# Kernel optimization log

Measured on AMD Instinct MI355X. Metric: run time of the kernel, lower is better.

## Reference

```python
import jax, jax.numpy as jnp
import numpy as np

N_NODES = 40000
N_EDGES = 640000
N_GRAPHS = 400
HID = 64
EDGE_DIM = 4
NUM_CLASSES = 12
EPS_BN = 1e-5


def _glorot(key, shape, fan_in, fan_out):
    s = jnp.sqrt(6.0 / (fan_in + fan_out)).astype(jnp.float32)
    return jax.random.uniform(key, shape, jnp.float32, -s, s)


def setup_inputs() -> dict:
    key = jax.random.key(0)
    ks = jax.random.split(key, 24)
    x = jax.random.normal(ks[0], (N_NODES, 2), jnp.float32)
    edge_index = jax.random.randint(ks[1], (2, N_EDGES), 0, N_NODES, jnp.int32)
    edge_attr = jax.random.normal(ks[2], (N_EDGES, EDGE_DIM), jnp.float32)
    batch = jnp.sort(jax.random.randint(ks[3], (N_NODES,), 0, N_GRAPHS, jnp.int32))
    H1, C1 = 4, HID            # conv1: heads=4, out=64, concat -> 256
    H2, C2 = 2, HID * 2        # conv2: heads=2, out=128, mean -> 128
    d1 = H1 * C1               # 256
    d2 = H2 * C2               # 256 (pre-mean), post 128
    return {
        "x": x, "edge_index": edge_index, "edge_attr": edge_attr, "batch": batch,
        # conv1 params
        "Wl1": _glorot(ks[4], (2, d1), 2, d1), "bl1": jnp.zeros((d1,), jnp.float32),
        "Wr1": _glorot(ks[5], (2, d1), 2, d1), "br1": jnp.zeros((d1,), jnp.float32),
        "We1": _glorot(ks[6], (EDGE_DIM, d1), EDGE_DIM, d1),
        "att1": _glorot(ks[7], (H1, C1), C1, 1),
        "bias1": jnp.zeros((d1,), jnp.float32),
        "g1": jnp.ones((d1,), jnp.float32), "be1": jnp.zeros((d1,), jnp.float32),
        # conv2 params
        "Wl2": _glorot(ks[8], (d1, d2), d1, d2), "bl2": jnp.zeros((d2,), jnp.float32),
        "Wr2": _glorot(ks[9], (d1, d2), d1, d2), "br2": jnp.zeros((d2,), jnp.float32),
        "We2": _glorot(ks[10], (EDGE_DIM, d2), EDGE_DIM, d2),
        "att2": _glorot(ks[11], (H2, C2), C2, 1),
        "bias2": jnp.zeros((C2,), jnp.float32),
        "g2": jnp.ones((C2,), jnp.float32), "be2": jnp.zeros((C2,), jnp.float32),
        # MLP head
        "W_lin1": _glorot(ks[12], (C2, HID), C2, HID), "b_lin1": jnp.zeros((HID,), jnp.float32),
        "W_lin2": _glorot(ks[13], (HID, NUM_CLASSES), HID, NUM_CLASSES),
        "b_lin2": jnp.zeros((NUM_CLASSES,), jnp.float32),
    }


def gatv2(x, src, dst, ea, Wl, bl, Wr, br, We, att, bias, heads, out_ch, concat):
    N = x.shape[0]
    xl = (x @ Wl + bl).reshape(N, heads, out_ch)   # source transform
    xr = (x @ Wr + br).reshape(N, heads, out_ch)   # target transform
    ee = (ea @ We).reshape(-1, heads, out_ch)      # edge features
    z = jax.nn.leaky_relu(xl[src] + xr[dst] + ee, 0.2)  # [E,H,C]
    e = jnp.einsum('ehc,hc->eh', z, att)
    # segment softmax over edges grouped by destination node
    m = jax.ops.segment_max(e, dst, num_segments=N)
    ex = jnp.exp(e - m[dst])
    den = jax.ops.segment_sum(ex, dst, num_segments=N)
    alpha = ex / (den[dst] + 1e-16)
    out = jax.ops.segment_sum(xl[src] * alpha[:, :, None], dst, num_segments=N)
    out = out.reshape(N, heads * out_ch) if concat else out.mean(axis=1)
    return out + bias


def batchnorm(x, g, b):
    mu = x.mean(axis=0)
    var = x.var(axis=0)
    return (x - mu) * jax.lax.rsqrt(var + EPS_BN) * g + b


def reference(x, edge_index, edge_attr, batch,
              Wl1, bl1, Wr1, br1, We1, att1, bias1, g1, be1,
              Wl2, bl2, Wr2, br2, We2, att2, bias2, g2, be2,
              W_lin1, b_lin1, W_lin2, b_lin2):
    src, dst = edge_index[0], edge_index[1]
    h = gatv2(x, src, dst, edge_attr, Wl1, bl1, Wr1, br1, We1, att1, bias1, 4, HID, True)
    h = jax.nn.elu(batchnorm(h, g1, be1))
    h = gatv2(h, src, dst, edge_attr, Wl2, bl2, Wr2, br2, We2, att2, bias2, 2, HID * 2, False)
    h = jax.nn.elu(batchnorm(h, g2, be2))
    # global mean pool per graph
    s = jax.ops.segment_sum(h, batch, num_segments=N_GRAPHS)
    cnt = jax.ops.segment_sum(jnp.ones((h.shape[0],), h.dtype), batch, num_segments=N_GRAPHS)
    h = s / jnp.maximum(cnt, 1.0)[:, None]
    h = jax.nn.elu(h @ W_lin1 + b_lin1)
    return h @ W_lin2 + b_lin2
```

## Files before the change

### kernel.cpp

```cpp
#include <hip/hip_runtime.h>
#include <math.h>

#define NN_ 40000
#define NE_ 640000
#define NG_ 400
#define NBLK_SCAN 157
#define NBP 1024
#define NB2 32

typedef unsigned short ushort_t;
typedef __attribute__((ext_vector_type(8))) short bf16x8;
typedef __attribute__((ext_vector_type(4))) float f32x4;

__device__ int    g_deg[NN_];
__device__ int    g_rowstart[NN_ + 1];
__device__ int    g_cursor[NN_];
__device__ int    g_srccsr[NE_];
__device__ float4 g_eacsr[NE_];
__device__ int    g_bsum[NBLK_SCAN], g_boff[NBLK_SCAN];
__device__ ushort_t g_xl1[(size_t)NN_ * 256];
__device__ ushort_t g_xr1[(size_t)NN_ * 256];
__device__ ushort_t g_xl2[(size_t)NN_ * 256];
__device__ ushort_t g_xr2[(size_t)NN_ * 256];
__device__ float  g_h1[(size_t)NN_ * 256];
__device__ ushort_t g_h1b[(size_t)NN_ * 256];
__device__ ushort_t g_wl2t[256 * 256];
__device__ ushort_t g_wr2t[256 * 256];
__device__ float  g_h2[(size_t)NN_ * 128];
__device__ float  g_part_s[NBP][256];
__device__ float  g_part_q[NBP][256];
__device__ float  g_p2_s[NB2][256];
__device__ float  g_p2_q[NB2][256];
__device__ float  g_scale[256], g_shift[256];
__device__ float  g_pool[NG_ * 128];
__device__ int    g_count[NG_];

__device__ __forceinline__ float bflo(unsigned int q) { return __uint_as_float(q << 16); }
__device__ __forceinline__ float bfhi(unsigned int q) { return __uint_as_float(q & 0xFFFF0000u); }
__device__ __forceinline__ unsigned int f2bf(float f) {
    unsigned int u = __float_as_uint(f);
    return (u + 0x7FFFu + ((u >> 16) & 1u)) >> 16;
}
__device__ __forceinline__ unsigned int pack2(float a, float b) {
    return f2bf(a) | (f2bf(b) << 16);
}

__global__ void k_zero() {
    int i = blockIdx.x * blockDim.x + threadIdx.x;
    int stride = gridDim.x * blockDim.x;
    for (int j = i; j < NN_; j += stride) g_deg[j] = 0;
}

__global__ void k_hist(const int* __restrict__ dst) {
    int e = blockIdx.x * blockDim.x + threadIdx.x;
    if (e < NE_) atomicAdd(&g_deg[dst[e]], 1);
}

__global__ void k_scan1() {
    __shared__ int sd[256];
    int b = blockIdx.x, t = threadIdx.x, i = b * 256 + t;
    int v = (i < NN_) ? g_deg[i] : 0;
    sd[t] = v;
    __syncthreads();
    for (int off = 1; off < 256; off <<= 1) {
        int tv = (t >= off) ? sd[t - off] : 0;
        __syncthreads();
        sd[t] += tv;
        __syncthreads();
    }
    if (i < NN_) g_rowstart[i] = sd[t] - v;
    if (t == 255) g_bsum[b] = sd[255];
}

__global__ void k_scan2() {
    __shared__ int sd[256];
    int t = threadIdx.x;
    int v = (t < NBLK_SCAN) ? g_bsum[t] : 0;
    sd[t] = v;
    __syncthreads();
    for (int off = 1; off < 256; off <<= 1) {
        int tv = (t >= off) ? sd[t - off] : 0;
        __syncthreads();
        sd[t] += tv;
        __syncthreads();
    }
    if (t < NBLK_SCAN) g_boff[t] = sd[t] - v;
    if (t == 255) g_rowstart[NN_] = sd[255];
}

__global__ void k_scan3() {
    int i = blockIdx.x * blockDim.x + threadIdx.x;
    if (i < NN_) {
        int r = g_rowstart[i] + g_boff[i >> 8];
        g_rowstart[i] = r;
        g_cursor[i] = r;
    }
}

__global__ void k_scatter(const int* __restrict__ src, const int* __restrict__ dst,
                          const float* __restrict__ ea) {
    int e = blockIdx.x * blockDim.x + threadIdx.x;
    if (e < NE_) {
        int pos = atomicAdd(&g_cursor[dst[e]], 1);
        g_srccsr[pos] = src[e];
        g_eacsr[pos] = reinterpret_cast<const float4*>(ea)[e];
    }
}

__global__ void k_xform1(const float* __restrict__ x,
                         const float* __restrict__ Wl, const float* __restrict__ bl,
                         const float* __restrict__ Wr, const float* __restrict__ br) {
    int n = blockIdx.x * 4 + (threadIdx.x >> 6);
    int lane = threadIdx.x & 63;
    if (n >= NN_) return;
    float x0 = x[2 * n], x1 = x[2 * n + 1];
    int c4 = lane * 4;
    float l0 = x0 * Wl[c4 + 0] + x1 * Wl[256 + c4 + 0] + bl[c4 + 0];
    float l1 = x0 * Wl[c4 + 1] + x1 * Wl[256 + c4 + 1] + bl[c4 + 1];
    float l2 = x0 * Wl[c4 + 2] + x1 * Wl[256 + c4 + 2] + bl[c4 + 2];
    float l3 = x0 * Wl[c4 + 3] + x1 * Wl[256 + c4 + 3] + bl[c4 + 3];
    float r0 = x0 * Wr[c4 + 0] + x1 * Wr[256 + c4 + 0] + br[c4 + 0];
    float r1 = x0 * Wr[c4 + 1] + x1 * Wr[256 + c4 + 1] + br[c4 + 1];
    float r2 = x0 * Wr[c4 + 2] + x1 * Wr[256 + c4 + 2] + br[c4 + 2];
    float r3 = x0 * Wr[c4 + 3] + x1 * Wr[256 + c4 + 3] + br[c4 + 3];
    *reinterpret_cast<uint2*>(g_xl1 + (size_t)n * 256 + c4) = make_uint2(pack2(l0, l1), pack2(l2, l3));
    *reinterpret_cast<uint2*>(g_xr1 + (size_t)n * 256 + c4) = make_uint2(pack2(r0, r1), pack2(r2, r3));
}

template <int LAYER>
__global__ void k_gat(const float* __restrict__ att, const float* __restrict__ We,
                      const float* __restrict__ bias) {
    constexpr int C = (LAYER == 1) ? 64 : 128;
    constexpr int GL = C / 4;
    const ushort_t* __restrict__ xl = (LAYER == 1) ? g_xl1 : g_xl2;
    const ushort_t* __restrict__ xr = (LAYER == 1) ? g_xr1 : g_xr2;
    float* __restrict__ hout = (LAYER == 1) ? g_h1 : g_h2;

    int wv = threadIdx.x >> 6, lane = threadIdx.x & 63;
    int n = blockIdx.x * 4 + wv;
    if (n >= NN_) return;
    int c4 = lane * 4;

    float a0 = att[c4], a1 = att[c4 + 1], a2c = att[c4 + 2], a3 = att[c4 + 3];
    float we00 = We[c4], we01 = We[c4 + 1], we02 = We[c4 + 2], we03 = We[c4 + 3];
    float we10 = We[256 + c4], we11 = We[256 + c4 + 1], we12 = We[256 + c4 + 2], we13 = We[256 + c4 + 3];
    float we20 = We[512 + c4], we21 = We[512 + c4 + 1], we22 = We[512 + c4 + 2], we23 = We[512 + c4 + 3];
    float we30 = We[768 + c4], we31 = We[768 + c4 + 1], we32 = We[768 + c4 + 2], we33 = We[768 + c4 + 3];
    uint2 xq = *reinterpret_cast<const uint2*>(xr + (size_t)n * 256 + c4);
    float xr0 = bflo(xq.x), xr1 = bfhi(xq.x), xr2 = bflo(xq.y), xr3 = bfhi(xq.y);

    int s0 = g_rowstart[n];
    int d = g_rowstart[n + 1] - s0;

    float mrun = -INFINITY, den = 0.f;
    float acc0 = 0.f, acc1 = 0.f, acc2 = 0.f, acc3 = 0.f;

    int   sA = 0;
    float4 eaA = make_float4(0.f, 0.f, 0.f, 0.f);
    uint2 rowA = make_uint2(0u, 0u);
    if (d > 0) {
        sA = g_srccsr[s0];
        eaA = g_eacsr[s0];
        rowA = *reinterpret_cast<const uint2*>(xl + (size_t)sA * 256 + c4);
    }
    for (int i = 0; i < d; ++i) {
        int   sB = sA;
        float4 eaB = eaA;
        uint2 rowB = rowA;
        if (i + 1 < d) {
            sB = g_srccsr[s0 + i + 1];
            eaB = g_eacsr[s0 + i + 1];
            rowB = *reinterpret_cast<const uint2*>(xl + (size_t)sB * 256 + c4);
        }
        float xl0 = bflo(rowA.x), xl1 = bfhi(rowA.x), xl2 = bflo(rowA.y), xl3 = bfhi(rowA.y);
        float z0 = xl0 + xr0 + eaA.x * we00 + eaA.y * we10 + eaA.z * we20 + eaA.w * we30;
        float z1 = xl1 + xr1 + eaA.x * we01 + eaA.y * we11 + eaA.z * we21 + eaA.w * we31;
        float z2 = xl2 + xr2 + eaA.x * we02 + eaA.y * we12 + eaA.z * we22 + eaA.w * we32;
        float z3 = xl3 + xr3 + eaA.x * we03 + eaA.y * we13 + eaA.z * we23 + eaA.w * we33;
        z0 = fmaxf(z0, 0.2f * z0); z1 = fmaxf(z1, 0.2f * z1);
        z2 = fmaxf(z2, 0.2f * z2); z3 = fmaxf(z3, 0.2f * z3);
        float t = z0 * a0 + z1 * a1 + z2 * a2c + z3 * a3;
#pragma unroll
        for (int off = 1; off < GL; off <<= 1) t += __shfl_xor(t, off);
        if (__ballot(t > mrun) == 0ULL) {
            float w = __expf(t - mrun);
            den += w;
            acc0 = fmaf(w, xl0, acc0);
            acc1 = fmaf(w, xl1, acc1);
            acc2 = fmaf(w, xl2, acc2);
            acc3 = fmaf(w, xl3, acc3);
        } else {
            float mnew = fmaxf(mrun, t);
            float scl = __expf(mrun - mnew);
            float w = __expf(t - mnew);
            den = den * scl + w;
            acc0 = acc0 * scl + w * xl0;
            acc1 = acc1 * scl + w * xl1;
            acc2 = acc2 * scl + w * xl2;
            acc3 = acc3 * scl + w * xl3;
            mrun = mnew;
        }
        sA = sB; eaA = eaB; rowA = rowB;
    }
    float inv = 1.f / (den + 1e-16f);
    if (LAYER == 1) {
        float4 o = make_float4(acc0 * inv + bias[c4 + 0], acc1 * inv + bias[c4 + 1],
                               acc2 * inv + bias[c4 + 2], acc3 * inv + bias[c4 + 3]);
        *reinterpret_cast<float4*>(hout + (size_t)n * 256 + c4) = o;
    } else {
        float v0 = acc0 * inv, v1 = acc1 * inv, v2 = acc2 * inv, v3 = acc3 * inv;
        float u0 = __shfl_xor(v0, 32), u1 = __shfl_xor(v1, 32);
        float u2 = __shfl_xor(v2, 32), u3 = __shfl_xor(v3, 32);
        if (lane < 32) {
            float4 o = make_float4(0.5f * (v0 + u0) + bias[c4 + 0],
                                   0.5f * (v1 + u1) + bias[c4 + 1],
                                   0.5f * (v2 + u2) + bias[c4 + 2],
                                   0.5f * (v3 + u3) + bias[c4 + 3]);
            *reinterpret_cast<float4*>(hout + (size_t)n * 128 + c4) = o;
        }
    }
}

template <int C>
__global__ void k_bn_stats() {
    const float* h = (C == 256) ? (const float*)g_h1 : (const float*)g_h2;
    int c = threadIdx.x;
    float s = 0.f, ss = 0.f;
    for (int r = blockIdx.x; r < NN_; r += NBP) {
        float v = h[(size_t)r * C + c];
        s += v; ss += v * v;
    }
    g_part_s[blockIdx.x][c] = s;
    g_part_q[blockIdx.x][c] = ss;
}

template <int C>
__global__ void k_bn_reduce() {
    int c = threadIdx.x;
    int b = blockIdx.x;
    float s = 0.f, ss = 0.f;
    for (int p = b; p < NBP; p += NB2) {
        s += g_part_s[p][c];
        ss += g_part_q[p][c];
    }
    g_p2_s[b][c] = s;
    g_p2_q[b][c] = ss;
}

template <int C>
__global__ void k_bn_finalize(const float* __restrict__ g, const float* __restrict__ b) {
    int c = threadIdx.x;
    float s = 0.f, ss = 0.f;
#pragma unroll
    for (int p = 0; p < NB2; ++p) {
        s += g_p2_s[p][c];
        ss += g_p2_q[p][c];
    }
    float mu = s / (float)NN_;
    float var = ss / (float)NN_ - mu * mu;
    float sc = g[c] * rsqrtf(var + 1e-5f);
    g_scale[c] = sc;
    g_shift[c] = b[c] - mu * sc;
}

__global__ void k_bn_apply1() {
    int i = blockIdx.x * blockDim.x + threadIdx.x;
    int stride = gridDim.x * blockDim.x;
    for (int j8 = i; j8 < NN_ * 32; j8 += stride) {
        size_t base = (size_t)j8 * 8;
        int c0 = (int)(base & 255);
        float4 v0 = *reinterpret_cast<const float4*>(g_h1 + base);
        float4 v1 = *reinterpret_cast<const float4*>(g_h1 + base + 4);
        float e[8];
        e[0] = v0.x * g_scale[c0 + 0] + g_shift[c0 + 0];
        e[1] = v0.y * g_scale[c0 + 1] + g_shift[c0 + 1];
        e[2] = v0.z * g_scale[c0 + 2] + g_shift[c0 + 2];
        e[3] = v0.w * g_scale[c0 + 3] + g_shift[c0 + 3];
        e[4] = v1.x * g_scale[c0 + 4] + g_shift[c0 + 4];
        e[5] = v1.y * g_scale[c0 + 5] + g_shift[c0 + 5];
        e[6] = v1.z * g_scale[c0 + 6] + g_shift[c0 + 6];
        e[7] = v1.w * g_scale[c0 + 7] + g_shift[c0 + 7];
#pragma unroll
        for (int q = 0; q < 8; ++q) e[q] = e[q] > 0.f ? e[q] : expm1f(e[q]);
        uint4 o = make_uint4(pack2(e[0], e[1]), pack2(e[2], e[3]),
                             pack2(e[4], e[5]), pack2(e[6], e[7]));
        *reinterpret_cast<uint4*>(g_h1b + base) = o;
    }
}

__global__ void k_wconv(const float* __restrict__ Wl, const float* __restrict__ Wr) {
    int n = blockIdx.x, k = threadIdx.x;
    g_wl2t[n * 256 + k] = (ushort_t)f2bf(Wl[(size_t)k * 256 + n]);
    g_wr2t[n * 256 + k] = (ushort_t)f2bf(Wr[(size_t)k * 256 + n]);
}

__global__ __launch_bounds__(256) void k_gemm2(const float* __restrict__ bl,
                                               const float* __restrict__ br) {
    __shared__ ushort_t As[128][40];
    __shared__ ushort_t Bs[2][64][40];
    int tid = threadIdx.x;
    int w = tid >> 6, lane = tid & 63;
    int m0 = blockIdx.x * 128, n0 = blockIdx.y * 64;

    f32x4 acc[2][4][2] = {};

    for (int k0 = 0; k0 < 256; k0 += 32) {
#pragma unroll
        for (int c = tid; c < 512; c += 256) {
            int row = c >> 2, seg = c & 3;
            int gr = m0 + row; gr = gr < NN_ ? gr : NN_ - 1;
            uint4 v = *reinterpret_cast<const uint4*>(g_h1b + (size_t)gr * 256 + k0 + seg * 8);
            *reinterpret_cast<uint4*>(&As[row][seg * 8]) = v;
        }
        {
            int row = tid >> 2, seg = tid & 3;
            uint4 v0 = *reinterpret_cast<const uint4*>(g_wl2t + (size_t)(n0 + row) * 256 + k0 + seg * 8);
            *reinterpret_cast<uint4*>(&Bs[0][row][seg * 8]) = v0;
            uint4 v1 = *reinterpret_cast<const uint4*>(g_wr2t + (size_t)(n0 + row) * 256 + k0 + seg * 8);
            *reinterpret_cast<uint4*>(&Bs[1][row][seg * 8]) = v1;
        }
        __syncthreads();
        int kb = (lane >> 4) * 8;
        bf16x8 a0 = *reinterpret_cast<const bf16x8*>(&As[w * 32 + (lane & 15)][kb]);
        bf16x8 a1 = *reinterpret_cast<const bf16x8*>(&As[w * 32 + 16 + (lane & 15)][kb]);
        bf16x8 b[4][2];
#pragma unroll
        for (int ni = 0; ni < 4; ++ni) {
            b[ni][0] = *reinterpret_cast<const bf16x8*>(&Bs[0][ni * 16 + (lane & 15)][kb]);
            b[ni][1] = *reinterpret_cast<const bf16x8*>(&Bs[1][ni * 16 + (lane & 15)][kb]);
        }
#pragma unroll
        for (int ni = 0; ni < 4; ++ni) {
#pragma unroll
            for (int mat = 0; mat < 2; ++mat) {
                acc[0][ni][mat] = __builtin_amdgcn_mfma_f32_16x16x32_bf16(a0, b[ni][mat], acc[0][ni][mat], 0, 0, 0);
                acc[1][ni][mat] = __builtin_amdgcn_mfma_f32_16x16x32_bf16(a1, b[ni][mat], acc[1][ni][mat], 0, 0, 0);
            }
        }
        __syncthreads();
    }
#pragma unroll
    for (int mat = 0; mat < 2; ++mat) {
        const float* bb = mat ? br : bl;
        ushort_t* outp = mat ? g_xr2 : g_xl2;
#pragma unroll
        for (int ni = 0; ni < 4; ++ni) {
            int gcol = n0 + ni * 16 + (lane & 15);
            float bv = bb[gcol];
#pragma unroll
            for (int mi = 0; mi < 2; ++mi) {
#pragma unroll
                for (int r = 0; r < 4; ++r) {
                    int grow = m0 + w * 32 + mi * 16 + (lane >> 4) * 4 + r;
                    if (grow < NN_)
                        outp[(size_t)grow * 256 + gcol] = (ushort_t)f2bf(acc[mi][ni][mat][r] + bv);
                }
            }
        }
    }
}

__global__ void k_pool2(const int* __restrict__ batch) {
    int g = blockIdx.x, t = threadIdx.x;
    __shared__ int sbeg, send;
    if (t == 0) {
        int lo = 0, hi = NN_;
        while (lo < hi) { int mid = (lo + hi) >> 1; if (batch[mid] < g) lo = mid + 1; else hi = mid; }
        sbeg = lo;
    }
    if (t == 1) {
        int lo = 0, hi = NN_;
        while (lo < hi) { int mid = (lo + hi) >> 1; if (batch[mid] <= g) lo = mid + 1; else hi = mid; }
        send = lo;
    }
    __syncthreads();
    int beg = sbeg, end = send;
    float sc = g_scale[t], sh = g_shift[t];
    float acc = 0.f;
    for (int n = beg; n < end; ++n) {
        float v = g_h2[(size_t)n * 128 + t] * sc + sh;
        acc += (v > 0.f ? v : expm1f(v));
    }
    g_pool[g * 128 + t] = acc;
    if (t == 0) g_count[g] = end - beg;
}

__global__ void k_head(const float* __restrict__ W1, const float* __restrict__ b1,
                       const float* __restrict__ W2, const float* __restrict__ b2,
                       float* __restrict__ out) {
    int g = blockIdx.x, t = threadIdx.x;
    __shared__ float p[128], hm[64];
    float cnt = fmaxf((float)g_count[g], 1.f);
    float inv = 1.f / cnt;
    p[t] = g_pool[g * 128 + t] * inv;
    p[t + 64] = g_pool[g * 128 + 64 + t] * inv;
    __syncthreads();
    float a = b1[t];
    for (int k = 0; k < 128; ++k) a += p[k] * W1[k * 64 + t];
    hm[t] = a > 0.f ? a : expm1f(a);
    __syncthreads();
    if (t < 12) {
        float o = b2[t];
        for (int k = 0; k < 64; ++k) o += hm[k] * W2[k * 12 + t];
        out[g * 12 + t] = o;
    }
}

extern "C" void kernel_launch(void* const* d_in, const int* in_sizes, int n_in,
                              void* d_out, int out_size, void* d_ws, size_t ws_size,
                              hipStream_t stream) {
    const float* x     = (const float*)d_in[0];
    const int*   ei    = (const int*)d_in[1];
    const float* ea    = (const float*)d_in[2];
    const int*   batch = (const int*)d_in[3];
    const float* Wl1   = (const float*)d_in[4];
    const float* bl1   = (const float*)d_in[5];
    const float* Wr1   = (const float*)d_in[6];
    const float* br1   = (const float*)d_in[7];
    const float* We1   = (const float*)d_in[8];
    const float* att1  = (const float*)d_in[9];
    const float* bias1 = (const float*)d_in[10];
    const float* g1    = (const float*)d_in[11];
    const float* be1   = (const float*)d_in[12];
    const float* Wl2   = (const float*)d_in[13];
    const float* bl2   = (const float*)d_in[14];
    const float* Wr2   = (const float*)d_in[15];
    const float* br2   = (const float*)d_in[16];
    const float* We2   = (const float*)d_in[17];
    const float* att2  = (const float*)d_in[18];
    const float* bias2 = (const float*)d_in[19];
    const float* g2    = (const float*)d_in[20];
    const float* be2   = (const float*)d_in[21];
    const float* Wlin1 = (const float*)d_in[22];
    const float* blin1 = (const float*)d_in[23];
    const float* Wlin2 = (const float*)d_in[24];
    const float* blin2 = (const float*)d_in[25];
    float* out = (float*)d_out;
    const int* src = ei;
    const int* dst = ei + NE_;

    k_zero<<<256, 256, 0, stream>>>();
    k_hist<<<2500, 256, 0, stream>>>(dst);
    k_scan1<<<NBLK_SCAN, 256, 0, stream>>>();
    k_scan2<<<1, 256, 0, stream>>>();
    k_scan3<<<NBLK_SCAN, 256, 0, stream>>>();
    k_scatter<<<2500, 256, 0, stream>>>(src, dst, ea);

    k_xform1<<<10000, 256, 0, stream>>>(x, Wl1, bl1, Wr1, br1);
    k_wconv<<<256, 256, 0, stream>>>(Wl2, Wr2);
    k_gat<1><<<10000, 256, 0, stream>>>(att1, We1, bias1);
    k_bn_stats<256><<<NBP, 256, 0, stream>>>();
    k_bn_reduce<256><<<NB2, 256, 0, stream>>>();
    k_bn_finalize<256><<<1, 256, 0, stream>>>(g1, be1);
    k_bn_apply1<<<2048, 256, 0, stream>>>();

    k_gemm2<<<dim3(313, 4), 256, 0, stream>>>(bl2, br2);

    k_gat<2><<<10000, 256, 0, stream>>>(att2, We2, bias2);
    k_bn_stats<128><<<NBP, 128, 0, stream>>>();
    k_bn_reduce<128><<<NB2, 128, 0, stream>>>();
    k_bn_finalize<128><<<1, 128, 0, stream>>>(g2, be2);

    k_pool2<<<NG_, 128, 0, stream>>>(batch);
    k_head<<<NG_, 64, 0, stream>>>(Wlin1, blin1, Wlin2, blin2, out);
}
```

Measured before the change: 473.2 us.

## Fuse layer-1 linear transform into GAT gather and merge BN2 finalize with pool and head

Layer 1 no longer materializes the 256-wide bf16 xl1/xr1 tensors. Each edge now gathers only the 2-float input x of its source node and recomputes the linear projection in registers. This removes a large write plus random 512-byte gathers per edge, at the cost of a few extra FMAs. Separately, the BN2 finalize, pooling and MLP head are merged into one kernel, which cuts two launches and some intermediate global buffers but repeats the BN stat reduction in every block.

```diff
diff --git a/kernel.cpp b/kernel.cpp
--- a/kernel.cpp
+++ b/kernel.cpp
@@ -18,8 +18,6 @@
 __device__ int    g_srccsr[NE_];
 __device__ float4 g_eacsr[NE_];
 __device__ int    g_bsum[NBLK_SCAN], g_boff[NBLK_SCAN];
-__device__ ushort_t g_xl1[(size_t)NN_ * 256];
-__device__ ushort_t g_xr1[(size_t)NN_ * 256];
 __device__ ushort_t g_xl2[(size_t)NN_ * 256];
 __device__ ushort_t g_xr2[(size_t)NN_ * 256];
 __device__ float  g_h1[(size_t)NN_ * 256];
@@ -32,8 +30,6 @@
 __device__ float  g_p2_s[NB2][256];
 __device__ float  g_p2_q[NB2][256];
 __device__ float  g_scale[256], g_shift[256];
-__device__ float  g_pool[NG_ * 128];
-__device__ int    g_count[NG_];
 
 __device__ __forceinline__ float bflo(unsigned int q) { return __uint_as_float(q << 16); }
 __device__ __forceinline__ float bfhi(unsigned int q) { return __uint_as_float(q & 0xFFFF0000u); }
@@ -107,33 +103,13 @@
     }
 }
 
-__global__ void k_xform1(const float* __restrict__ x,
-                         const float* __restrict__ Wl, const float* __restrict__ bl,
-                         const float* __restrict__ Wr, const float* __restrict__ br) {
-    int n = blockIdx.x * 4 + (threadIdx.x >> 6);
-    int lane = threadIdx.x & 63;
-    if (n >= NN_) return;
-    float x0 = x[2 * n], x1 = x[2 * n + 1];
-    int c4 = lane * 4;
-    float l0 = x0 * Wl[c4 + 0] + x1 * Wl[256 + c4 + 0] + bl[c4 + 0];
-    float l1 = x0 * Wl[c4 + 1] + x1 * Wl[256 + c4 + 1] + bl[c4 + 1];
-    float l2 = x0 * Wl[c4 + 2] + x1 * Wl[256 + c4 + 2] + bl[c4 + 2];
-    float l3 = x0 * Wl[c4 + 3] + x1 * Wl[256 + c4 + 3] + bl[c4 + 3];
-    float r0 = x0 * Wr[c4 + 0] + x1 * Wr[256 + c4 + 0] + br[c4 + 0];
-    float r1 = x0 * Wr[c4 + 1] + x1 * Wr[256 + c4 + 1] + br[c4 + 1];
-    float r2 = x0 * Wr[c4 + 2] + x1 * Wr[256 + c4 + 2] + br[c4 + 2];
-    float r3 = x0 * Wr[c4 + 3] + x1 * Wr[256 + c4 + 3] + br[c4 + 3];
-    *reinterpret_cast<uint2*>(g_xl1 + (size_t)n * 256 + c4) = make_uint2(pack2(l0, l1), pack2(l2, l3));
-    *reinterpret_cast<uint2*>(g_xr1 + (size_t)n * 256 + c4) = make_uint2(pack2(r0, r1), pack2(r2, r3));
-}
-
 template <int LAYER>
 __global__ void k_gat(const float* __restrict__ att, const float* __restrict__ We,
-                      const float* __restrict__ bias) {
+                      const float* __restrict__ bias, const float* __restrict__ x,
+                      const float* __restrict__ Wl, const float* __restrict__ bl,
+                      const float* __restrict__ Wr, const float* __restrict__ br) {
     constexpr int C = (LAYER == 1) ? 64 : 128;
     constexpr int GL = C / 4;
-    const ushort_t* __restrict__ xl = (LAYER == 1) ? g_xl1 : g_xl2;
-    const ushort_t* __restrict__ xr = (LAYER == 1) ? g_xr1 : g_xr2;
     float* __restrict__ hout = (LAYER == 1) ? g_h1 : g_h2;
 
     int wv = threadIdx.x >> 6, lane = threadIdx.x & 63;
@@ -146,8 +122,24 @@
     float we10 = We[256 + c4], we11 = We[256 + c4 + 1], we12 = We[256 + c4 + 2], we13 = We[256 + c4 + 3];
     float we20 = We[512 + c4], we21 = We[512 + c4 + 1], we22 = We[512 + c4 + 2], we23 = We[512 + c4 + 3];
     float we30 = We[768 + c4], we31 = We[768 + c4 + 1], we32 = We[768 + c4 + 2], we33 = We[768 + c4 + 3];
-    uint2 xq = *reinterpret_cast<const uint2*>(xr + (size_t)n * 256 + c4);
-    float xr0 = bflo(xq.x), xr1 = bfhi(xq.x), xr2 = bflo(xq.y), xr3 = bfhi(xq.y);
+
+    float wl00 = 0.f, wl01 = 0.f, wl02 = 0.f, wl03 = 0.f;
+    float wl10 = 0.f, wl11 = 0.f, wl12 = 0.f, wl13 = 0.f;
+    float bl0 = 0.f, bl1 = 0.f, bl2 = 0.f, bl3 = 0.f;
+    float xr0, xr1, xr2, xr3;
+    if constexpr (LAYER == 1) {
+        wl00 = Wl[c4 + 0]; wl01 = Wl[c4 + 1]; wl02 = Wl[c4 + 2]; wl03 = Wl[c4 + 3];
+        wl10 = Wl[256 + c4 + 0]; wl11 = Wl[256 + c4 + 1]; wl12 = Wl[256 + c4 + 2]; wl13 = Wl[256 + c4 + 3];
+        bl0 = bl[c4 + 0]; bl1 = bl[c4 + 1]; bl2 = bl[c4 + 2]; bl3 = bl[c4 + 3];
+        float2 xn = *reinterpret_cast<const float2*>(x + 2 * n);
+        xr0 = xn.x * Wr[c4 + 0] + xn.y * Wr[256 + c4 + 0] + br[c4 + 0];
+        xr1 = xn.x * Wr[c4 + 1] + xn.y * Wr[256 + c4 + 1] + br[c4 + 1];
+        xr2 = xn.x * Wr[c4 + 2] + xn.y * Wr[256 + c4 + 2] + br[c4 + 2];
+        xr3 = xn.x * Wr[c4 + 3] + xn.y * Wr[256 + c4 + 3] + br[c4 + 3];
+    } else {
+        uint2 xq = *reinterpret_cast<const uint2*>(g_xr2 + (size_t)n * 256 + c4);
+        xr0 = bflo(xq.x); xr1 = bfhi(xq.x); xr2 = bflo(xq.y); xr3 = bfhi(xq.y);
+    }
 
     int s0 = g_rowstart[n];
     int d = g_rowstart[n + 1] - s0;
@@ -155,24 +147,34 @@
     float mrun = -INFINITY, den = 0.f;
     float acc0 = 0.f, acc1 = 0.f, acc2 = 0.f, acc3 = 0.f;
 
-    int   sA = 0;
     float4 eaA = make_float4(0.f, 0.f, 0.f, 0.f);
-    uint2 rowA = make_uint2(0u, 0u);
+    float2 xsA = make_float2(0.f, 0.f);
+    uint2  rowA = make_uint2(0u, 0u);
     if (d > 0) {
-        sA = g_srccsr[s0];
+        int sA = g_srccsr[s0];
         eaA = g_eacsr[s0];
-        rowA = *reinterpret_cast<const uint2*>(xl + (size_t)sA * 256 + c4);
+        if constexpr (LAYER == 1) xsA = *reinterpret_cast<const float2*>(x + 2 * sA);
+        else rowA = *reinterpret_cast<const uint2*>(g_xl2 + (size_t)sA * 256 + c4);
     }
     for (int i = 0; i < d; ++i) {
-        int   sB = sA;
         float4 eaB = eaA;
-        uint2 rowB = rowA;
+        float2 xsB = xsA;
+        uint2  rowB = rowA;
         if (i + 1 < d) {
-            sB = g_srccsr[s0 + i + 1];
+            int sB = g_srccsr[s0 + i + 1];
             eaB = g_eacsr[s0 + i + 1];
-            rowB = *reinterpret_cast<const uint2*>(xl + (size_t)sB * 256 + c4);
-        }
-        float xl0 = bflo(rowA.x), xl1 = bfhi(rowA.x), xl2 = bflo(rowA.y), xl3 = bfhi(rowA.y);
+            if constexpr (LAYER == 1) xsB = *reinterpret_cast<const float2*>(x + 2 * sB);
+            else rowB = *reinterpret_cast<const uint2*>(g_xl2 + (size_t)sB * 256 + c4);
+        }
+        float xl0, xl1, xl2, xl3;
+        if constexpr (LAYER == 1) {
+            xl0 = fmaf(xsA.y, wl10, fmaf(xsA.x, wl00, bl0));
+            xl1 = fmaf(xsA.y, wl11, fmaf(xsA.x, wl01, bl1));
+            xl2 = fmaf(xsA.y, wl12, fmaf(xsA.x, wl02, bl2));
+            xl3 = fmaf(xsA.y, wl13, fmaf(xsA.x, wl03, bl3));
+        } else {
+            xl0 = bflo(rowA.x); xl1 = bfhi(rowA.x); xl2 = bflo(rowA.y); xl3 = bfhi(rowA.y);
+        }
         float z0 = xl0 + xr0 + eaA.x * we00 + eaA.y * we10 + eaA.z * we20 + eaA.w * we30;
         float z1 = xl1 + xr1 + eaA.x * we01 + eaA.y * we11 + eaA.z * we21 + eaA.w * we31;
         float z2 = xl2 + xr2 + eaA.x * we02 + eaA.y * we12 + eaA.z * we22 + eaA.w * we32;
@@ -200,10 +202,10 @@
             acc3 = acc3 * scl + w * xl3;
             mrun = mnew;
         }
-        sA = sB; eaA = eaB; rowA = rowB;
+        eaA = eaB; xsA = xsB; rowA = rowB;
     }
     float inv = 1.f / (den + 1e-16f);
-    if (LAYER == 1) {
+    if constexpr (LAYER == 1) {
         float4 o = make_float4(acc0 * inv + bias[c4 + 0], acc1 * inv + bias[c4 + 1],
                                acc2 * inv + bias[c4 + 2], acc3 * inv + bias[c4 + 3]);
         *reinterpret_cast<float4*>(hout + (size_t)n * 256 + c4) = o;
@@ -360,8 +362,22 @@
     }
 }
 
-__global__ void k_pool2(const int* __restrict__ batch) {
+__global__ void k_tail(const float* __restrict__ g2, const float* __restrict__ be2,
+                       const int* __restrict__ batch,
+                       const float* __restrict__ W1, const float* __restrict__ b1,
+                       const float* __restrict__ W2, const float* __restrict__ b2,
+                       float* __restrict__ out) {
     int g = blockIdx.x, t = threadIdx.x;
+    float s = 0.f, ss = 0.f;
+#pragma unroll
+    for (int p = 0; p < NB2; ++p) {
+        s += g_p2_s[p][t];
+        ss += g_p2_q[p][t];
+    }
+    float mu = s / (float)NN_;
+    float var = ss / (float)NN_ - mu * mu;
+    float sc = g2[t] * rsqrtf(var + 1e-5f);
+    float sh = be2[t] - mu * sc;
     __shared__ int sbeg, send;
     if (t == 0) {
         int lo = 0, hi = NN_;
@@ -375,29 +391,20 @@
     }
     __syncthreads();
     int beg = sbeg, end = send;
-    float sc = g_scale[t], sh = g_shift[t];
     float acc = 0.f;
     for (int n = beg; n < end; ++n) {
         float v = g_h2[(size_t)n * 128 + t] * sc + sh;
         acc += (v > 0.f ? v : expm1f(v));
     }
-    g_pool[g * 128 + t] = acc;
-    if (t == 0) g_count[g] = end - beg;
-}
-
-__global__ void k_head(const float* __restrict__ W1, const float* __restrict__ b1,
-                       const float* __restrict__ W2, const float* __restrict__ b2,
-                       float* __restrict__ out) {
-    int g = blockIdx.x, t = threadIdx.x;
     __shared__ float p[128], hm[64];
-    float cnt = fmaxf((float)g_count[g], 1.f);
-    float inv = 1.f / cnt;
-    p[t] = g_pool[g * 128 + t] * inv;
-    p[t + 64] = g_pool[g * 128 + 64 + t] * inv;
+    float cnt = fmaxf((float)(end - beg), 1.f);
+    p[t] = acc / cnt;
     __syncthreads();
-    float a = b1[t];
-    for (int k = 0; k < 128; ++k) a += p[k] * W1[k * 64 + t];
-    hm[t] = a > 0.f ? a : expm1f(a);
+    if (t < 64) {
+        float a = b1[t];
+        for (int k = 0; k < 128; ++k) a += p[k] * W1[k * 64 + t];
+        hm[t] = a > 0.f ? a : expm1f(a);
+    }
     __syncthreads();
     if (t < 12) {
         float o = b2[t];
@@ -446,9 +453,8 @@
     k_scan3<<<NBLK_SCAN, 256, 0, stream>>>();
     k_scatter<<<2500, 256, 0, stream>>>(src, dst, ea);
 
-    k_xform1<<<10000, 256, 0, stream>>>(x, Wl1, bl1, Wr1, br1);
     k_wconv<<<256, 256, 0, stream>>>(Wl2, Wr2);
-    k_gat<1><<<10000, 256, 0, stream>>>(att1, We1, bias1);
+    k_gat<1><<<10000, 256, 0, stream>>>(att1, We1, bias1, x, Wl1, bl1, Wr1, br1);
     k_bn_stats<256><<<NBP, 256, 0, stream>>>();
     k_bn_reduce<256><<<NB2, 256, 0, stream>>>();
     k_bn_finalize<256><<<1, 256, 0, stream>>>(g1, be1);
@@ -456,11 +462,9 @@
 
     k_gemm2<<<dim3(313, 4), 256, 0, stream>>>(bl2, br2);
 
-    k_gat<2><<<10000, 256, 0, stream>>>(att2, We2, bias2);
+    k_gat<2><<<10000, 256, 0, stream>>>(att2, We2, bias2, x, Wl1, bl1, Wr1, br1);
     k_bn_stats<128><<<NBP, 128, 0, stream>>>();
     k_bn_reduce<128><<<NB2, 128, 0, stream>>>();
-    k_bn_finalize<128><<<1, 128, 0, stream>>>(g2, be2);
-
-    k_pool2<<<NG_, 128, 0, stream>>>(batch);
-    k_head<<<NG_, 64, 0, stream>>>(Wlin1, blin1, Wlin2, blin2, out);
-}
+
+    k_tail<<<NG_, 128, 0, stream>>>(g2, be2, batch, Wlin1, blin1, Wlin2, blin2, out);
+}
```

New measurement: 459.9 us. 2.8% less time.
